# Kernel tuning notes

Hardware: AMD Instinct MI355X
Metric: run time of the kernel (lower is better)

## Reference

```python
import jax, jax.numpy as jnp
import numpy as np

WINDOW = 8
HEADS = 16
HIDDEN = 256
EMBED = HIDDEN * WINDOW          # 2048
HEAD_DIM = EMBED // HEADS        # 128
BATCH = 8
SEQ = 4096                       # multiple of WINDOW
GROUP = SEQ // WINDOW            # 512


def _indices():
    # index_one[i*g + j] = j*w + i  (residue-class grouping permutation)
    i = np.arange(WINDOW)
    j = np.arange(GROUP)
    index_one = (j[None, :] * WINDOW + i[:, None]).reshape(-1)
    # index_two[i*w + k] = k*g + i  (inverse-style interleave permutation)
    index_two = (np.arange(WINDOW)[None, :] * GROUP + np.arange(GROUP)[:, None]).reshape(-1)
    return jnp.asarray(index_one), jnp.asarray(index_two)


def _attention(M, Wq, Wk, Wv, fc_w, fc_b):
    # M: [N, g, E] with E = heads*head_dim
    N, L, E = M.shape
    x = M.reshape(N, L, HEADS, HEAD_DIM)
    q = jnp.einsum('nlhd,ed->nlhe', x, Wq)
    k = jnp.einsum('nlhd,ed->nlhe', x, Wk)
    v = jnp.einsum('nlhd,ed->nlhe', x, Wv)
    energy = jnp.einsum('nqhd,nkhd->nhqk', q, k)
    attn = jax.nn.softmax(energy / jnp.sqrt(jnp.float32(EMBED)), axis=-1)
    out = jnp.einsum('nhqk,nkhd->nqhd', attn, v).reshape(N, L, E)
    return out @ fc_w.T + fc_b


def setup_inputs() -> dict:
    key = jax.random.key(0)
    ks = jax.random.split(key, 6)
    s = 0.02
    return {
        'M': jax.random.normal(ks[0], (BATCH, SEQ, HIDDEN), jnp.float32),
        'Wq': jax.random.normal(ks[1], (HEAD_DIM, HEAD_DIM), jnp.float32) * s,
        'Wk': jax.random.normal(ks[2], (HEAD_DIM, HEAD_DIM), jnp.float32) * s,
        'Wv': jax.random.normal(ks[3], (HEAD_DIM, HEAD_DIM), jnp.float32) * s,
        'fc_w': jax.random.normal(ks[4], (EMBED, EMBED), jnp.float32) * s,
        'fc_b': jax.random.normal(ks[5], (EMBED,), jnp.float32) * s,
        'device': 0,
    }


def reference(M, Wq, Wk, Wv, fc_w, fc_b, device):
    del device  # unused, mirrors torch signature
    index_one, index_two = _indices()
    N, S, H = M.shape
    w, g = WINDOW, GROUP
    for b in range(w):
        idx = (index_one - b) % S
        M = M[:, idx]                                             # gather permute
        # segmentation step 1: [N, w*g, H] -> [N, g, w*H]
        M = M.reshape(N, w, g, H).transpose(0, 2, 1, 3).reshape(N, g, w * H)
        M = _attention(M, Wq, Wk, Wv, fc_w, fc_b)
        # segmentation step 2: [N, g, w*H] -> [N, w*g, H]
        M = M.reshape(N, g, w, H).transpose(0, 2, 1, 3).reshape(N, w * g, H)
        # index_two rotated once per iteration after the first -> roll by -b
        M = M[:, jnp.roll(index_two, -b)]
    return M[:, :S]
```

## Files before the change

### kernel.cpp

```cpp
#include <hip/hip_runtime.h>
#include <stdint.h>

typedef unsigned short u16;
typedef unsigned int u32;
typedef __bf16 bf16x8 __attribute__((ext_vector_type(8)));
typedef float f32x4 __attribute__((ext_vector_type(4)));
typedef float f32x16 __attribute__((ext_vector_type(16)));
typedef u16 u16x4 __attribute__((ext_vector_type(4)));
typedef u16 u16x8 __attribute__((ext_vector_type(8)));

#define MFMA16(a, b, c) __builtin_amdgcn_mfma_f32_16x16x32_bf16(a, b, c, 0, 0, 0)
#define MFMA32(a, b, c) __builtin_amdgcn_mfma_f32_32x32x16_bf16(a, b, c, 0, 0, 0)

__device__ __forceinline__ u16 f2bf(float f) {
  u32 u = __builtin_bit_cast(u32, f);
  u += 0x7FFFu + ((u >> 16) & 1u);
  return (u16)(u >> 16);
}

__device__ __forceinline__ bf16x8 ld16(const u16* p) {
  return __builtin_bit_cast(bf16x8, *(const uint4*)p);
}

__device__ __forceinline__ void gl_lds(const u16* src, u16* lds) {
  __builtin_amdgcn_global_load_lds(
      (const __attribute__((address_space(1))) u32*)src,
      (__attribute__((address_space(3))) u32*)lds, 16, 0, 0);
}

__global__ __launch_bounds__(256) void convert_weights(
    const float* __restrict__ Wq, const float* __restrict__ Wk,
    const float* __restrict__ Wv, const float* __restrict__ fcw,
    u16* __restrict__ wq_b, u16* __restrict__ wk_b, u16* __restrict__ wv_b,
    u16* __restrict__ fcw_b) {
  int bx = blockIdx.x, tid = threadIdx.x;
  if (bx < 4096) {
    int i = (bx * 256 + tid) * 4;
    float4 f = *(const float4*)&fcw[i];
    u16x4 o = {f2bf(f.x), f2bf(f.y), f2bf(f.z), f2bf(f.w)};
    *(u16x4*)&fcw_b[i] = o;
  } else {
    int i = ((bx - 4096) * 256 + tid) * 4;
    const float sc = 0.022097086912079612f;
    float4 q = *(const float4*)&Wq[i];
    u16x4 oq = {f2bf(q.x * sc), f2bf(q.y * sc), f2bf(q.z * sc), f2bf(q.w * sc)};
    *(u16x4*)&wq_b[i] = oq;
    float4 k = *(const float4*)&Wk[i];
    u16x4 ok = {f2bf(k.x), f2bf(k.y), f2bf(k.z), f2bf(k.w)};
    *(u16x4*)&wk_b[i] = ok;
    float4 v = *(const float4*)&Wv[i];
    u16x4 ov = {f2bf(v.x), f2bf(v.y), f2bf(v.z), f2bf(v.w)};
    *(u16x4*)&wv_b[i] = ov;
  }
}

__global__ __launch_bounds__(768) void qkv_kernel(
    const float* __restrict__ srcF, const u16* __restrict__ srcB, int srcf32,
    const u16* __restrict__ wq, const u16* __restrict__ wk,
    const u16* __restrict__ wvw, u16* __restrict__ Q, u16* __restrict__ K,
    u16* __restrict__ Vt, int bsh) {
  __shared__ u16 X[64 * 264];
  int jt = blockIdx.x, i0 = blockIdx.y, n = blockIdx.z;
  int tid = threadIdx.x;
#pragma unroll
  for (int it = 0; it < 3; ++it) {
    int c = tid + it * 768;
    if (c < 2048) {
      int row = c >> 5, seg = c & 31;
      int pos = (8 * (jt * 64 + row) + i0 - bsh) & 4095;
      size_t base = ((size_t)n * 4096 + pos) * 256 + seg * 8;
      if (srcf32) {
        float4 f0 = *(const float4*)&srcF[base];
        float4 f1 = *(const float4*)&srcF[base + 4];
        u16x8 v = {f2bf(f0.x), f2bf(f0.y), f2bf(f0.z), f2bf(f0.w),
                   f2bf(f1.x), f2bf(f1.y), f2bf(f1.z), f2bf(f1.w)};
        *(u16x8*)&X[row * 264 + seg * 8] = v;
      } else {
        *(u16x8*)&X[row * 264 + seg * 8] = *(const u16x8*)&srcB[base];
      }
    }
  }
  __syncthreads();
  int wvid = tid >> 6, ln = tid & 63;
  int mat = wvid >> 2, hc = wvid & 3;
  int hh = hc >> 1, cb = (hc & 1) * 64;
  int h = i0 * 2 + hh, xc = hh * 128;
  const u16* W = (mat == 0) ? wq : (mat == 1) ? wk : wvw;
  int lr = ln & 15, lg = ln >> 4;
  f32x4 acc[4][4] = {};
#pragma unroll
  for (int kt = 0; kt < 4; ++kt) {
    bf16x8 a[4], b[4];
#pragma unroll
    for (int mt = 0; mt < 4; ++mt)
      a[mt] = ld16(&X[(mt * 16 + lr) * 264 + xc + kt * 32 + lg * 8]);
#pragma unroll
    for (int nc = 0; nc < 4; ++nc)
      b[nc] = ld16(&W[(cb + nc * 16 + lr) * 128 + kt * 32 + lg * 8]);
#pragma unroll
    for (int mt = 0; mt < 4; ++mt)
#pragma unroll
      for (int nc = 0; nc < 4; ++nc)
        acc[mt][nc] = MFMA16(a[mt], b[nc], acc[mt][nc]);
  }
  size_t nh = (size_t)(n * 16 + h);
  if (mat < 2) {
    u16* dst = (mat == 0 ? Q : K) + nh * 512 * 128;
#pragma unroll
    for (int mt = 0; mt < 4; ++mt)
#pragma unroll
      for (int nc = 0; nc < 4; ++nc) {
        int col = cb + nc * 16 + lr;
        int jb = jt * 64 + mt * 16 + lg * 4;
#pragma unroll
        for (int r = 0; r < 4; ++r)
          dst[(size_t)(jb + r) * 128 + col] = f2bf(acc[mt][nc][r]);
      }
  } else {
    u16* dst = Vt + nh * 128 * 512;
#pragma unroll
    for (int mt = 0; mt < 4; ++mt)
#pragma unroll
      for (int nc = 0; nc < 4; ++nc) {
        int col = cb + nc * 16 + lr;
        int jb = jt * 64 + mt * 16 + lg * 4;
        u16x4 pk = {f2bf(acc[mt][nc][0]), f2bf(acc[mt][nc][1]),
                    f2bf(acc[mt][nc][2]), f2bf(acc[mt][nc][3])};
        *(u16x4*)&dst[(size_t)col * 512 + jb] = pk;
      }
  }
}

__global__ __launch_bounds__(256, 2) void attn_kernel(
    const u16* __restrict__ Q, const u16* __restrict__ K,
    const u16* __restrict__ Vt, u16* __restrict__ O) {
  __shared__ u16 KL[3][64 * 128];
  __shared__ u16 VL[2][128 * 64];
  int flat = blockIdx.x;
  int xcd = flat & 7, idx = flat >> 3;
  int gl = idx & 15, qt = idx >> 4;
  int g = xcd | (gl << 3);
  int h = g & 15, n = g >> 4;
  int tid = threadIdx.x, wv = tid >> 6, ln = tid & 63;
  int l31 = ln & 31, hh = ln >> 5;
  size_t nh = (size_t)(n * 16 + h);
  int q0 = qt * 128 + wv * 32;
  const u16* Qb = Q + ((size_t)nh * 512 + q0) * 128;
  const u16* Kb = K + (size_t)nh * 512 * 128;
  const u16* Vb = Vt + (size_t)nh * 128 * 512;

  bf16x8 qf[8];
#pragma unroll
  for (int kt = 0; kt < 8; ++kt)
    qf[kt] = ld16(&Qb[l31 * 128 + kt * 16 + hh * 8]);

  int l16 = ln & 15, l8 = ln & 7;
  int rK[4], cK[4], rV[4], cV[4];
#pragma unroll
  for (int i = 0; i < 4; ++i) {
    int s = wv * 4 + i;
    rK[i] = 4 * s + (ln >> 4);
    cK[i] = (l16 ^ (rK[i] & 15)) * 8;
    rV[i] = 8 * s + (ln >> 3);
    cV[i] = (l8 ^ (rV[i] & 7)) * 8;
  }

#define STAGE_K(buf, kv)                                                     \
  {                                                                          \
    const u16* kp_ = Kb + (size_t)(kv) * 64 * 128;                           \
    _Pragma("unroll") for (int i_ = 0; i_ < 4; ++i_) {                       \
      int s_ = wv * 4 + i_;                                                  \
      gl_lds(&kp_[(size_t)rK[i_] * 128 + cK[i_]], &KL[buf][s_ * 512]);       \
    }                                                                        \
  }
#define STAGE_V(buf, kv)                                                     \
  {                                                                          \
    _Pragma("unroll") for (int i_ = 0; i_ < 4; ++i_) {                       \
      int s_ = wv * 4 + i_;                                                  \
      gl_lds(&Vb[(size_t)rV[i_] * 512 + (kv)*64 + cV[i_]], &VL[buf][s_ * 512]); \
    }                                                                        \
  }

  STAGE_K(0, 0);
  STAGE_V(0, 0);
  STAGE_K(1, 1);
  __syncthreads();

  f32x16 ps[2][2];
  f32x16 o[4] = {};
  float m = -1e30f, l = 0.f;

  {
    f32x16 z = {};
    ps[0][0] = z; ps[0][1] = z;
#pragma unroll
    for (int kt = 0; kt < 8; ++kt) {
      int slot0 = (2 * kt + hh) ^ (l31 & 15);
      bf16x8 a0 = ld16(&KL[0][l31 * 128 + slot0 * 8]);
      ps[0][0] = MFMA32(a0, qf[kt], ps[0][0]);
      int row1 = 32 + l31;
      int slot1 = (2 * kt + hh) ^ (row1 & 15);
      bf16x8 a1 = ld16(&KL[0][row1 * 128 + slot1 * 8]);
      ps[0][1] = MFMA32(a1, qf[kt], ps[0][1]);
    }
  }

#pragma unroll
  for (int t = 0; t < 8; ++t) {
    const int cur = t & 1, nxt = (t + 1) & 1;
    if (t + 2 <= 7) STAGE_K((t + 2) % 3, t + 2);
    if (t + 1 <= 7) STAGE_V(nxt, t + 1);
    if (t + 1 <= 7) {
      const int kb = (t + 1) % 3;
      f32x16 z = {};
      ps[nxt][0] = z; ps[nxt][1] = z;
#pragma unroll
      for (int kt = 0; kt < 8; ++kt) {
        int slot0 = (2 * kt + hh) ^ (l31 & 15);
        bf16x8 a0 = ld16(&KL[kb][l31 * 128 + slot0 * 8]);
        ps[nxt][0] = MFMA32(a0, qf[kt], ps[nxt][0]);
        int row1 = 32 + l31;
        int slot1 = (2 * kt + hh) ^ (row1 & 15);
        bf16x8 a1 = ld16(&KL[kb][row1 * 128 + slot1 * 8]);
        ps[nxt][1] = MFMA32(a1, qf[kt], ps[nxt][1]);
      }
    }
    float mx[8];
#pragma unroll
    for (int i = 0; i < 8; ++i)
      mx[i] = fmaxf(fmaxf(ps[cur][0][2 * i], ps[cur][0][2 * i + 1]),
                    fmaxf(ps[cur][1][2 * i], ps[cur][1][2 * i + 1]));
    float pm = fmaxf(fmaxf(fmaxf(mx[0], mx[1]), fmaxf(mx[2], mx[3])),
                     fmaxf(fmaxf(mx[4], mx[5]), fmaxf(mx[6], mx[7])));
    pm = fmaxf(pm, __shfl_xor(pm, 32));
    if (!__all(pm <= m + 8.f)) {
      float nm = fmaxf(m, pm);
      float al = __expf(m - nm);
      l *= al;
      m = nm;
#pragma unroll
      for (int r = 0; r < 16; ++r) {
        int qr = (r & 3) + 8 * (r >> 2) + 4 * hh;
        float av = __shfl(al, (ln & 32) | qr, 64);
        o[0][r] *= av; o[1][r] *= av; o[2][r] *= av; o[3][r] *= av;
      }
    }
#pragma unroll
    for (int kb2 = 0; kb2 < 2; ++kb2)
#pragma unroll
      for (int r = 0; r < 16; ++r)
        ps[cur][kb2][r] = __expf(ps[cur][kb2][r] - m);
    float sm[8];
#pragma unroll
    for (int i = 0; i < 8; ++i)
      sm[i] = (ps[cur][0][2 * i] + ps[cur][0][2 * i + 1]) +
              (ps[cur][1][2 * i] + ps[cur][1][2 * i + 1]);
    float rs = ((sm[0] + sm[1]) + (sm[2] + sm[3])) +
               ((sm[4] + sm[5]) + (sm[6] + sm[7]));
    rs += __shfl_xor(rs, 32);
    l += rs;
    bf16x8 pa[4];
#pragma unroll
    for (int ks = 0; ks < 4; ++ks) {
      const int kb2 = ks >> 1, r0 = 8 * (ks & 1);
      u32 wA, wB, wC, wD;
      asm("v_cvt_pk_bf16_f32 %0, %1, %2" : "=v"(wA) : "v"(ps[cur][kb2][r0 + 0]), "v"(ps[cur][kb2][r0 + 1]));
      asm("v_cvt_pk_bf16_f32 %0, %1, %2" : "=v"(wB) : "v"(ps[cur][kb2][r0 + 2]), "v"(ps[cur][kb2][r0 + 3]));
      asm("v_cvt_pk_bf16_f32 %0, %1, %2" : "=v"(wC) : "v"(ps[cur][kb2][r0 + 4]), "v"(ps[cur][kb2][r0 + 5]));
      asm("v_cvt_pk_bf16_f32 %0, %1, %2" : "=v"(wD) : "v"(ps[cur][kb2][r0 + 6]), "v"(ps[cur][kb2][r0 + 7]));
      asm("v_permlane32_swap_b32 %0, %1" : "+v"(wA), "+v"(wC));
      asm("v_permlane32_swap_b32 %0, %1" : "+v"(wB), "+v"(wD));
      uint4 ww = {wA, wB, wC, wD};
      pa[ks] = __builtin_bit_cast(bf16x8, ww);
    }
    __builtin_amdgcn_s_setprio(1);
#pragma unroll
    for (int ks = 0; ks < 4; ++ks)
#pragma unroll
      for (int nb = 0; nb < 4; ++nb) {
        int row = nb * 32 + l31;
        int slot = (2 * ks + hh) ^ (row & 7);
        bf16x8 bv = ld16(&VL[cur][row * 64 + slot * 8]);
        o[nb] = MFMA32(pa[ks], bv, o[nb]);
      }
    __builtin_amdgcn_s_setprio(0);
    if (t < 7) __syncthreads();
  }
#undef STAGE_K
#undef STAGE_V

  float inv = 1.f / l;
#pragma unroll
  for (int r = 0; r < 16; ++r) {
    int qr = (r & 3) + 8 * (r >> 2) + 4 * hh;
    float iv = __shfl(inv, (ln & 32) | qr, 64);
    int row = q0 + qr;
    u16* dst = O + ((size_t)n * 512 + row) * 2048 + h * 128;
    dst[0 * 32 + l31] = f2bf(o[0][r] * iv);
    dst[1 * 32 + l31] = f2bf(o[1][r] * iv);
    dst[2 * 32 + l31] = f2bf(o[2][r] * iv);
    dst[3 * 32 + l31] = f2bf(o[3][r] * iv);
  }
}

__global__ __launch_bounds__(256, 2) void fc_kernel(
    const u16* __restrict__ A, const u16* __restrict__ Bw,
    const float* __restrict__ bias, float* __restrict__ doutF,
    u16* __restrict__ doutB, int last, int bsh) {
  __shared__ u16 AL[2][128 * 64];
  __shared__ u16 BL[2][128 * 64];
  int bn = blockIdx.x, bm = blockIdx.y;
  int tid = threadIdx.x, wv = tid >> 6, ln = tid & 63;
  int lr = ln & 15, lg = ln >> 4;
  int R0 = bm * 128, C0 = bn * 128;
  int wr = (wv & 1) * 64, wc = (wv >> 1) * 64;
  const u16 *gAsrc[4], *gBsrc[4];
  int srow[4];
#pragma unroll
  for (int i = 0; i < 4; ++i) {
    int r = i * 32 + wv * 8 + (ln >> 3);
    int cs = ((ln & 7) ^ (r & 7)) * 8;
    gAsrc[i] = A + (size_t)(R0 + r) * 2048 + cs;
    gBsrc[i] = Bw + (size_t)(C0 + r) * 2048 + cs;
    srow[i] = i * 32 + wv * 8;
  }
  int aoff[4][2], boff[4][2];
#pragma unroll
  for (int i = 0; i < 4; ++i) {
    int ra = wr + i * 16 + lr, rb = wc + i * 16 + lr;
#pragma unroll
    for (int kk = 0; kk < 2; ++kk) {
      aoff[i][kk] = ra * 64 + (((kk * 4 + lg) ^ (ra & 7)) * 8);
      boff[i][kk] = rb * 64 + (((kk * 4 + lg) ^ (rb & 7)) * 8);
    }
  }
  f32x4 acc[4][4] = {};
#pragma unroll
  for (int i = 0; i < 4; ++i) {
    gl_lds(gAsrc[i], &AL[0][srow[i] * 64]);
    gl_lds(gBsrc[i], &BL[0][srow[i] * 64]);
  }
  for (int t = 0; t < 32; ++t) {
    int cur = t & 1, nx = cur ^ 1;
    if (t < 31) {
      int k0 = (t + 1) * 64;
#pragma unroll
      for (int i = 0; i < 4; ++i) {
        gl_lds(gAsrc[i] + k0, &AL[nx][srow[i] * 64]);
        gl_lds(gBsrc[i] + k0, &BL[nx][srow[i] * 64]);
      }
      asm volatile("s_waitcnt vmcnt(8)" ::: "memory");
    } else {
      asm volatile("s_waitcnt vmcnt(0)" ::: "memory");
    }
    __builtin_amdgcn_s_barrier();
#pragma unroll
    for (int kk = 0; kk < 2; ++kk) {
      bf16x8 a[4], b[4];
#pragma unroll
      for (int i = 0; i < 4; ++i) a[i] = ld16(&AL[cur][aoff[i][kk]]);
#pragma unroll
      for (int i = 0; i < 4; ++i) b[i] = ld16(&BL[cur][boff[i][kk]]);
      __builtin_amdgcn_s_setprio(1);
#pragma unroll
      for (int mt = 0; mt < 4; ++mt)
#pragma unroll
        for (int nc = 0; nc < 4; ++nc)
          acc[mt][nc] = MFMA16(a[mt], b[nc], acc[mt][nc]);
      __builtin_amdgcn_s_setprio(0);
    }
    if (t < 31) __builtin_amdgcn_s_barrier();
  }
#pragma unroll
  for (int nc = 0; nc < 4; ++nc) {
    int e = C0 + wc + nc * 16 + lr;
    float bv = bias[e];
    int i = e >> 8, cc = e & 255;
#pragma unroll
    for (int mt = 0; mt < 4; ++mt)
#pragma unroll
      for (int r = 0; r < 4; ++r) {
        int row = R0 + wr + mt * 16 + lg * 4 + r;
        int nn = row >> 9, j = row & 511;
        int pos = (8 * j + i - bsh) & 4095;
        size_t di = ((size_t)nn * 4096 + pos) * 256 + cc;
        float v = acc[mt][nc][r] + bv;
        if (last) doutF[di] = v;
        else doutB[di] = f2bf(v);
      }
  }
}

extern "C" void kernel_launch(void* const* d_in, const int* in_sizes, int n_in,
                              void* d_out, int out_size, void* d_ws, size_t ws_size,
                              hipStream_t stream) {
  const float* M = (const float*)d_in[0];
  const float* Wq = (const float*)d_in[1];
  const float* Wk = (const float*)d_in[2];
  const float* Wv = (const float*)d_in[3];
  const float* fcw = (const float*)d_in[4];
  const float* fcb = (const float*)d_in[5];
  float* out = (float*)d_out;
  char* ws = (char*)d_ws;
  u16* wq_b = (u16*)(ws + (0 << 10));
  u16* wk_b = (u16*)(ws + (32 << 10));
  u16* wv_b = (u16*)(ws + (64 << 10));
  u16* fcw_b = (u16*)(ws + (128 << 10));
  u16* Qb = (u16*)(ws + ((size_t)16 << 20));
  u16* Kb = (u16*)(ws + ((size_t)32 << 20));
  u16* Vtb = (u16*)(ws + ((size_t)48 << 20));
  u16* Ab = (u16*)(ws + ((size_t)64 << 20));
  u16* Sb = (u16*)(ws + ((size_t)96 << 20));

  convert_weights<<<4112, 256, 0, stream>>>(Wq, Wk, Wv, fcw, wq_b, wk_b, wv_b, fcw_b);
  for (int b = 0; b < 8; ++b) {
    qkv_kernel<<<dim3(8, 8, 8), 768, 0, stream>>>(M, Sb, (b == 0) ? 1 : 0,
                                                  wq_b, wk_b, wv_b, Qb, Kb, Vtb, b);
    attn_kernel<<<512, 256, 0, stream>>>(Qb, Kb, Vtb, Ab);
    fc_kernel<<<dim3(16, 32), 256, 0, stream>>>(Ab, fcw_b, fcb, out, Sb,
                                                (b == 7) ? 1 : 0, b);
  }
}
```

Before: 721.2 us.

## Restructure FC GEMM into 256x128 tiles with triple-buffered interleaved pipeline and XCD mapping

The FC GEMM kernel moves to 512-thread blocks computing 256x128 tiles with a 1D grid of 256 blocks. Blocks are remapped so that neighbouring column tiles land on the same XCD, aiming to improve L2 reuse of the weight matrix. The K loop is now triple-buffered: global-to-LDS loads for step t+2 are split into two halves and interleaved between the two MFMA phases, separated by explicit barriers and sched_barrier. This trades more LDS use, lower occupancy (one block per CU) and extra barriers for better overlap of memory and MFMA work and better weight reuse.

```diff
diff --git a/kernel.cpp b/kernel.cpp
--- a/kernel.cpp
+++ b/kernel.cpp
@@ -303,26 +303,36 @@
   }
 }
 
-__global__ __launch_bounds__(256, 2) void fc_kernel(
+__global__ __launch_bounds__(512, 1) void fc_kernel(
     const u16* __restrict__ A, const u16* __restrict__ Bw,
     const float* __restrict__ bias, float* __restrict__ doutF,
     u16* __restrict__ doutB, int last, int bsh) {
-  __shared__ u16 AL[2][128 * 64];
-  __shared__ u16 BL[2][128 * 64];
-  int bn = blockIdx.x, bm = blockIdx.y;
+  __shared__ u16 AL[3][256 * 64];
+  __shared__ u16 BL[3][128 * 64];
+  int blk = blockIdx.x;
+  int xcd = blk & 7, j = blk >> 3;
+  int bn = xcd * 2 + (j & 1), bm = j >> 1;
   int tid = threadIdx.x, wv = tid >> 6, ln = tid & 63;
   int lr = ln & 15, lg = ln >> 4;
-  int R0 = bm * 128, C0 = bn * 128;
-  int wr = (wv & 1) * 64, wc = (wv >> 1) * 64;
-  const u16 *gAsrc[4], *gBsrc[4];
-  int srow[4];
+  int R0 = bm * 256, C0 = bn * 128;
+  int wr = (wv >> 1) * 64, wc = (wv & 1) * 64;
+  const u16* gA[4];
+  int sA[4];
+  const u16* gB[2];
+  int sB[2];
 #pragma unroll
   for (int i = 0; i < 4; ++i) {
-    int r = i * 32 + wv * 8 + (ln >> 3);
+    int r = wv * 32 + i * 8 + (ln >> 3);
     int cs = ((ln & 7) ^ (r & 7)) * 8;
-    gAsrc[i] = A + (size_t)(R0 + r) * 2048 + cs;
-    gBsrc[i] = Bw + (size_t)(C0 + r) * 2048 + cs;
-    srow[i] = i * 32 + wv * 8;
+    gA[i] = A + (size_t)(R0 + r) * 2048 + cs;
+    sA[i] = (wv * 32 + i * 8) * 64;
+  }
+#pragma unroll
+  for (int i = 0; i < 2; ++i) {
+    int r = wv * 16 + i * 8 + (ln >> 3);
+    int cs = ((ln & 7) ^ (r & 7)) * 8;
+    gB[i] = Bw + (size_t)(C0 + r) * 2048 + cs;
+    sB[i] = (wv * 16 + i * 8) * 64;
   }
   int aoff[4][2], boff[4][2];
 #pragma unroll
@@ -335,42 +345,92 @@
     }
   }
   f32x4 acc[4][4] = {};
-#pragma unroll
-  for (int i = 0; i < 4; ++i) {
-    gl_lds(gAsrc[i], &AL[0][srow[i] * 64]);
-    gl_lds(gBsrc[i], &BL[0][srow[i] * 64]);
-  }
+
+#define STAGE6(buf, k0)                          \
+  {                                              \
+    gl_lds(gA[0] + (k0), &AL[buf][sA[0]]);       \
+    gl_lds(gA[1] + (k0), &AL[buf][sA[1]]);       \
+    gl_lds(gA[2] + (k0), &AL[buf][sA[2]]);       \
+    gl_lds(gA[3] + (k0), &AL[buf][sA[3]]);       \
+    gl_lds(gB[0] + (k0), &BL[buf][sB[0]]);       \
+    gl_lds(gB[1] + (k0), &BL[buf][sB[1]]);       \
+  }
+
+  STAGE6(0, 0);
+  STAGE6(1, 64);
+  asm volatile("s_waitcnt vmcnt(6)" ::: "memory");
+  __builtin_amdgcn_s_barrier();
+
   for (int t = 0; t < 32; ++t) {
-    int cur = t & 1, nx = cur ^ 1;
-    if (t < 31) {
-      int k0 = (t + 1) * 64;
-#pragma unroll
-      for (int i = 0; i < 4; ++i) {
-        gl_lds(gAsrc[i] + k0, &AL[nx][srow[i] * 64]);
-        gl_lds(gBsrc[i] + k0, &BL[nx][srow[i] * 64]);
-      }
-      asm volatile("s_waitcnt vmcnt(8)" ::: "memory");
-    } else {
+    int cur = t % 3, nx2 = (t + 2) % 3;
+    int k2 = (t + 2) * 64;
+    bf16x8 a0 = ld16(&AL[cur][aoff[0][0]]), a1 = ld16(&AL[cur][aoff[1][0]]);
+    bf16x8 a2 = ld16(&AL[cur][aoff[2][0]]), a3 = ld16(&AL[cur][aoff[3][0]]);
+    bf16x8 b0 = ld16(&BL[cur][boff[0][0]]), b1 = ld16(&BL[cur][boff[1][0]]);
+    bf16x8 b2 = ld16(&BL[cur][boff[2][0]]), b3 = ld16(&BL[cur][boff[3][0]]);
+    if (t < 30) {
+      gl_lds(gA[0] + k2, &AL[nx2][sA[0]]);
+      gl_lds(gA[1] + k2, &AL[nx2][sA[1]]);
+      gl_lds(gB[0] + k2, &BL[nx2][sB[0]]);
+    }
+    __builtin_amdgcn_s_barrier();
+    asm volatile("s_waitcnt lgkmcnt(0)" ::: "memory");
+    __builtin_amdgcn_sched_barrier(0);
+    __builtin_amdgcn_s_setprio(1);
+    acc[0][0] = MFMA16(a0, b0, acc[0][0]);
+    acc[0][1] = MFMA16(a0, b1, acc[0][1]);
+    acc[0][2] = MFMA16(a0, b2, acc[0][2]);
+    acc[0][3] = MFMA16(a0, b3, acc[0][3]);
+    acc[1][0] = MFMA16(a1, b0, acc[1][0]);
+    acc[1][1] = MFMA16(a1, b1, acc[1][1]);
+    acc[1][2] = MFMA16(a1, b2, acc[1][2]);
+    acc[1][3] = MFMA16(a1, b3, acc[1][3]);
+    acc[2][0] = MFMA16(a2, b0, acc[2][0]);
+    acc[2][1] = MFMA16(a2, b1, acc[2][1]);
+    acc[2][2] = MFMA16(a2, b2, acc[2][2]);
+    acc[2][3] = MFMA16(a2, b3, acc[2][3]);
+    acc[3][0] = MFMA16(a3, b0, acc[3][0]);
+    acc[3][1] = MFMA16(a3, b1, acc[3][1]);
+    acc[3][2] = MFMA16(a3, b2, acc[3][2]);
+    acc[3][3] = MFMA16(a3, b3, acc[3][3]);
+    __builtin_amdgcn_s_setprio(0);
+    __builtin_amdgcn_s_barrier();
+    a0 = ld16(&AL[cur][aoff[0][1]]); a1 = ld16(&AL[cur][aoff[1][1]]);
+    a2 = ld16(&AL[cur][aoff[2][1]]); a3 = ld16(&AL[cur][aoff[3][1]]);
+    b0 = ld16(&BL[cur][boff[0][1]]); b1 = ld16(&BL[cur][boff[1][1]]);
+    b2 = ld16(&BL[cur][boff[2][1]]); b3 = ld16(&BL[cur][boff[3][1]]);
+    if (t < 30) {
+      gl_lds(gA[2] + k2, &AL[nx2][sA[2]]);
+      gl_lds(gA[3] + k2, &AL[nx2][sA[3]]);
+      gl_lds(gB[1] + k2, &BL[nx2][sB[1]]);
+      asm volatile("s_waitcnt vmcnt(6)" ::: "memory");
+    } else if (t == 30) {
       asm volatile("s_waitcnt vmcnt(0)" ::: "memory");
     }
     __builtin_amdgcn_s_barrier();
-#pragma unroll
-    for (int kk = 0; kk < 2; ++kk) {
-      bf16x8 a[4], b[4];
-#pragma unroll
-      for (int i = 0; i < 4; ++i) a[i] = ld16(&AL[cur][aoff[i][kk]]);
-#pragma unroll
-      for (int i = 0; i < 4; ++i) b[i] = ld16(&BL[cur][boff[i][kk]]);
-      __builtin_amdgcn_s_setprio(1);
-#pragma unroll
-      for (int mt = 0; mt < 4; ++mt)
-#pragma unroll
-        for (int nc = 0; nc < 4; ++nc)
-          acc[mt][nc] = MFMA16(a[mt], b[nc], acc[mt][nc]);
-      __builtin_amdgcn_s_setprio(0);
-    }
-    if (t < 31) __builtin_amdgcn_s_barrier();
-  }
+    asm volatile("s_waitcnt lgkmcnt(0)" ::: "memory");
+    __builtin_amdgcn_sched_barrier(0);
+    __builtin_amdgcn_s_setprio(1);
+    acc[0][0] = MFMA16(a0, b0, acc[0][0]);
+    acc[0][1] = MFMA16(a0, b1, acc[0][1]);
+    acc[0][2] = MFMA16(a0, b2, acc[0][2]);
+    acc[0][3] = MFMA16(a0, b3, acc[0][3]);
+    acc[1][0] = MFMA16(a1, b0, acc[1][0]);
+    acc[1][1] = MFMA16(a1, b1, acc[1][1]);
+    acc[1][2] = MFMA16(a1, b2, acc[1][2]);
+    acc[1][3] = MFMA16(a1, b3, acc[1][3]);
+    acc[2][0] = MFMA16(a2, b0, acc[2][0]);
+    acc[2][1] = MFMA16(a2, b1, acc[2][1]);
+    acc[2][2] = MFMA16(a2, b2, acc[2][2]);
+    acc[2][3] = MFMA16(a2, b3, acc[2][3]);
+    acc[3][0] = MFMA16(a3, b0, acc[3][0]);
+    acc[3][1] = MFMA16(a3, b1, acc[3][1]);
+    acc[3][2] = MFMA16(a3, b2, acc[3][2]);
+    acc[3][3] = MFMA16(a3, b3, acc[3][3]);
+    __builtin_amdgcn_s_setprio(0);
+    __builtin_amdgcn_s_barrier();
+  }
+#undef STAGE6
 #pragma unroll
   for (int nc = 0; nc < 4; ++nc) {
     int e = C0 + wc + nc * 16 + lr;
@@ -381,8 +441,8 @@
 #pragma unroll
       for (int r = 0; r < 4; ++r) {
         int row = R0 + wr + mt * 16 + lg * 4 + r;
-        int nn = row >> 9, j = row & 511;
-        int pos = (8 * j + i - bsh) & 4095;
+        int nn = row >> 9, jj = row & 511;
+        int pos = (8 * jj + i - bsh) & 4095;
         size_t di = ((size_t)nn * 4096 + pos) * 256 + cc;
         float v = acc[mt][nc][r] + bv;
         if (last) doutF[di] = v;
@@ -417,7 +477,7 @@
     qkv_kernel<<<dim3(8, 8, 8), 768, 0, stream>>>(M, Sb, (b == 0) ? 1 : 0,
                                                   wq_b, wk_b, wv_b, Qb, Kb, Vtb, b);
     attn_kernel<<<512, 256, 0, stream>>>(Qb, Kb, Vtb, Ab);
-    fc_kernel<<<dim3(16, 32), 256, 0, stream>>>(Ab, fcw_b, fcb, out, Sb,
-                                                (b == 7) ? 1 : 0, b);
-  }
-}
+    fc_kernel<<<256, 512, 0, stream>>>(Ab, fcw_b, fcb, out, Sb,
+                                       (b == 7) ? 1 : 0, b);
+  }
+}
```

Measured after the change: 714.0 us. About the same (-1.0%).
